# Performance work log

Hardware: AMD Instinct MI355X
Metric: run time of the kernel (lower is better)

Reference implementation:

```python
import jax, jax.numpy as jnp
import numpy as np

MEMORY_SIZE = 100000
FEATURE_DIM = 1024
BATCH = 4096


def setup_inputs() -> dict:
    key = jax.random.key(0)
    k1, k2, k3 = jax.random.split(key, 3)
    return {
        "features": jax.random.normal(k1, (BATCH, FEATURE_DIM), dtype=jnp.float32),
        "predictions": jax.random.normal(k2, (BATCH, FEATURE_DIM), dtype=jnp.float32),
        "confidences": jax.random.uniform(k3, (BATCH,), dtype=jnp.float32),
        "memory_features": jnp.zeros((MEMORY_SIZE, FEATURE_DIM), dtype=jnp.float32),
        "memory_predictions": jnp.zeros((MEMORY_SIZE, FEATURE_DIM), dtype=jnp.float32),
        "memory_confidences": jnp.ones((MEMORY_SIZE,), dtype=jnp.float32),
        "memory_index": 12345,
        "memory_full": 0,
    }


def reference(features, predictions, confidences,
              memory_features, memory_predictions, memory_confidences,
              memory_index, memory_full):
    # Vectorized equivalent of the per-sample circular-buffer write loop.
    M, D = memory_features.shape
    B = features.shape[0]
    # Slots written by the loop: (memory_index + i) % M for i in range(B).
    # B <= M so all indices are unique and .at[].set matches sequential writes.
    idx = (memory_index + jnp.arange(B)) % M  # [B]
    new_feat = memory_features.at[idx].set(features)
    new_pred = memory_predictions.at[idx].set(predictions)
    new_conf = memory_confidences.at[idx].set(confidences)
    new_index = (memory_index + B) % M
    wrapped = (memory_index + B) >= M  # loop hit memory_index == 0 at least once
    full = jnp.logical_or(jnp.asarray(memory_full, dtype=bool), jnp.asarray(wrapped))
    utilization = jnp.where(full, jnp.float32(1.0),
                            jnp.float32(new_index) / jnp.float32(M))
    conf_mean = confidences.mean()
    return new_feat, new_pred, new_conf, conf_mean, utilization
```

## Files before the change

### kernel.cpp

```cpp
#include <hip/hip_runtime.h>

__global__ void copy_update_rows(const float4* __restrict__ mem,
                                 const float4* __restrict__ batch,
                                 float4* __restrict__ out,
                                 const int* __restrict__ d_mi,
                                 int M, int B, int D4) {
    int row = blockIdx.x;
    int col = threadIdx.x;
    int rel = row - *d_mi;
    if (rel < 0) rel += M;
    unsigned g = (unsigned)row * (unsigned)D4 + (unsigned)col;
    if (rel < B) {
        out[g] = batch[(unsigned)rel * (unsigned)D4 + (unsigned)col];
    } else {
        out[g] = mem[g];
    }
}

__global__ void copy_update_conf(const float* __restrict__ mem,
                                 const float* __restrict__ batch,
                                 float* __restrict__ out,
                                 const int* __restrict__ d_mi,
                                 int M, int B) {
    int i = blockIdx.x * blockDim.x + threadIdx.x;
    if (i >= M) return;
    int rel = i - *d_mi;
    if (rel < 0) rel += M;
    out[i] = (rel < B) ? batch[rel] : mem[i];
}

__global__ void mean_and_util(const float* __restrict__ conf,
                              const int* __restrict__ d_mi,
                              const int* __restrict__ d_full,
                              float* __restrict__ out_mean,
                              float* __restrict__ out_util,
                              int B, int M) {
    __shared__ float warp_sums[8];
    float s = 0.0f;
    for (int i = threadIdx.x; i < B; i += blockDim.x) s += conf[i];
    #pragma unroll
    for (int off = 32; off > 0; off >>= 1) s += __shfl_down(s, off);
    int lane = threadIdx.x & 63;
    int wave = threadIdx.x >> 6;
    if (lane == 0) warp_sums[wave] = s;
    __syncthreads();
    if (threadIdx.x == 0) {
        int nwaves = (blockDim.x + 63) >> 6;
        float total = 0.0f;
        for (int w = 0; w < nwaves; ++w) total += warp_sums[w];
        out_mean[0] = total / (float)B;

        int mi = *d_mi;
        int ni = (mi + B) % M;
        bool wrapped = (mi + B) >= M;
        bool full = (*d_full != 0) || wrapped;
        out_util[0] = full ? 1.0f : (float)ni / (float)M;
    }
}

extern "C" void kernel_launch(void* const* d_in, const int* in_sizes, int n_in,
                              void* d_out, int out_size, void* d_ws, size_t ws_size,
                              hipStream_t stream) {
    const float* features     = (const float*)d_in[0];
    const float* predictions  = (const float*)d_in[1];
    const float* confidences  = (const float*)d_in[2];
    const float* mem_feat     = (const float*)d_in[3];
    const float* mem_pred     = (const float*)d_in[4];
    const float* mem_conf     = (const float*)d_in[5];
    const int*   d_mi         = (const int*)d_in[6];
    const int*   d_full       = (const int*)d_in[7];

    const int B  = in_sizes[2];
    const int MD = in_sizes[3];
    const int M  = in_sizes[5];
    const int D  = MD / M;
    const int D4 = D / 4;

    float* out       = (float*)d_out;
    float* out_feat  = out;
    float* out_pred  = out + (size_t)MD;
    float* out_conf  = out + (size_t)2 * MD;
    float* out_mean  = out_conf + M;
    float* out_util  = out_mean + 1;

    copy_update_rows<<<M, D4, 0, stream>>>((const float4*)mem_feat,
                                           (const float4*)features,
                                           (float4*)out_feat, d_mi, M, B, D4);
    copy_update_rows<<<M, D4, 0, stream>>>((const float4*)mem_pred,
                                           (const float4*)predictions,
                                           (float4*)out_pred, d_mi, M, B, D4);
    copy_update_conf<<<(M + 255) / 256, 256, 0, stream>>>(mem_conf, confidences,
                                                          out_conf, d_mi, M, B);
    mean_and_util<<<1, 256, 0, stream>>>(confidences, d_mi, d_full,
                                         out_mean, out_util, B, M);
}
```

Measured before the change: 1.250 ms.

## Fuse feature, prediction and confidence copies into one grid-stride nontemporal kernel

Replaces the three separate copy kernels (two row-copy, one confidence) with a single persistent grid-stride kernel of 2048 blocks. Each iteration copies both feature and prediction vectors, unrolled by two, and uses nontemporal loads and stores to avoid polluting the cache on this streaming copy of about 800 MB. This removes launch overhead and the tiny 256-thread row blocks, at the cost of per-element index arithmetic and a fixed grid size.

```diff
diff --git a/kernel.cpp b/kernel.cpp
--- a/kernel.cpp
+++ b/kernel.cpp
@@ -1,32 +1,54 @@
 #include <hip/hip_runtime.h>
 
-__global__ void copy_update_rows(const float4* __restrict__ mem,
-                                 const float4* __restrict__ batch,
-                                 float4* __restrict__ out,
-                                 const int* __restrict__ d_mi,
-                                 int M, int B, int D4) {
-    int row = blockIdx.x;
-    int col = threadIdx.x;
-    int rel = row - *d_mi;
-    if (rel < 0) rel += M;
-    unsigned g = (unsigned)row * (unsigned)D4 + (unsigned)col;
-    if (rel < B) {
-        out[g] = batch[(unsigned)rel * (unsigned)D4 + (unsigned)col];
-    } else {
-        out[g] = mem[g];
+typedef float f32x4 __attribute__((ext_vector_type(4)));
+
+__global__ __launch_bounds__(256)
+void fused_update(const f32x4* __restrict__ memf,
+                  const f32x4* __restrict__ memp,
+                  const f32x4* __restrict__ batf,
+                  const f32x4* __restrict__ batp,
+                  f32x4* __restrict__ outf,
+                  f32x4* __restrict__ outp,
+                  const float* __restrict__ memc,
+                  const float* __restrict__ batc,
+                  float* __restrict__ outc,
+                  const int* __restrict__ d_mi,
+                  int M, int B, int D4, int shift, int total4) {
+    const int mi = *d_mi;
+    const int stride = gridDim.x * blockDim.x;
+    const int tid0 = blockIdx.x * blockDim.x + threadIdx.x;
+
+    for (int c = tid0; c < M; c += stride) {
+        int rel = c - mi; if (rel < 0) rel += M;
+        const float* src = (rel < B) ? (batc + rel) : (memc + c);
+        __builtin_nontemporal_store(__builtin_nontemporal_load(src), outc + c);
     }
-}
 
-__global__ void copy_update_conf(const float* __restrict__ mem,
-                                 const float* __restrict__ batch,
-                                 float* __restrict__ out,
-                                 const int* __restrict__ d_mi,
-                                 int M, int B) {
-    int i = blockIdx.x * blockDim.x + threadIdx.x;
-    if (i >= M) return;
-    int rel = i - *d_mi;
-    if (rel < 0) rel += M;
-    out[i] = (rel < B) ? batch[rel] : mem[i];
+    const int mask = D4 - 1;
+
+#define BODY(G)                                                              \
+    {                                                                        \
+        int g_ = (G);                                                        \
+        int row_, off_;                                                      \
+        if (shift >= 0) { row_ = g_ >> shift; off_ = g_ & mask; }            \
+        else            { row_ = g_ / D4;     off_ = g_ - row_ * D4; }       \
+        int rel_ = row_ - mi; if (rel_ < 0) rel_ += M;                       \
+        int s_ = rel_ * D4 + off_;                                           \
+        const f32x4* sf_ = (rel_ < B) ? (batf + s_) : (memf + g_);           \
+        const f32x4* sp_ = (rel_ < B) ? (batp + s_) : (memp + g_);           \
+        f32x4 vf_ = __builtin_nontemporal_load(sf_);                         \
+        f32x4 vp_ = __builtin_nontemporal_load(sp_);                         \
+        __builtin_nontemporal_store(vf_, outf + g_);                         \
+        __builtin_nontemporal_store(vp_, outp + g_);                         \
+    }
+
+    int g = tid0;
+    for (; g + stride < total4; g += 2 * stride) {
+        BODY(g)
+        BODY(g + stride)
+    }
+    if (g < total4) BODY(g)
+#undef BODY
 }
 
 __global__ void mean_and_util(const float* __restrict__ conf,
@@ -75,6 +97,8 @@
     const int M  = in_sizes[5];
     const int D  = MD / M;
     const int D4 = D / 4;
+    const int total4 = M * D4;
+    const int shift  = ((D4 & (D4 - 1)) == 0) ? __builtin_ctz(D4) : -1;
 
     float* out       = (float*)d_out;
     float* out_feat  = out;
@@ -83,14 +107,15 @@
     float* out_mean  = out_conf + M;
     float* out_util  = out_mean + 1;
 
-    copy_update_rows<<<M, D4, 0, stream>>>((const float4*)mem_feat,
-                                           (const float4*)features,
-                                           (float4*)out_feat, d_mi, M, B, D4);
-    copy_update_rows<<<M, D4, 0, stream>>>((const float4*)mem_pred,
-                                           (const float4*)predictions,
-                                           (float4*)out_pred, d_mi, M, B, D4);
-    copy_update_conf<<<(M + 255) / 256, 256, 0, stream>>>(mem_conf, confidences,
-                                                          out_conf, d_mi, M, B);
+    const int blocks = 2048;
+
+    fused_update<<<blocks, 256, 0, stream>>>(
+        (const f32x4*)mem_feat, (const f32x4*)mem_pred,
+        (const f32x4*)features, (const f32x4*)predictions,
+        (f32x4*)out_feat, (f32x4*)out_pred,
+        mem_conf, confidences, out_conf,
+        d_mi, M, B, D4, shift, total4);
+
     mean_and_util<<<1, 256, 0, stream>>>(confidences, d_mi, d_full,
                                          out_mean, out_util, B, M);
 }
```

Measured after the change: 1.291 ms. 3.3% more time.
